# Kernel tuning notes

Hardware: AMD Instinct MI355X
Metric: run time of the kernel (lower is better)

Reference implementation:

```python
import jax, jax.numpy as jnp
import numpy as np

N_HEAD = 12
D_HEAD = 64  # key_dim // n_head = 768 // 12


def sparsemax(z):
    # Martins & Astudillo (2016): projection of each row of z onto the simplex.
    K = z.shape[-1]
    z_sorted = -jnp.sort(-z, axis=-1)                      # descending sort
    cs = jnp.cumsum(z_sorted, axis=-1)
    r = jnp.arange(1, K + 1, dtype=z.dtype)
    support = (1.0 + r * z_sorted) > cs                    # support set indicator
    ksz = jnp.sum(support, axis=-1, keepdims=True)         # support size k(z)
    cs_k = jnp.take_along_axis(cs, ksz.astype(jnp.int32) - 1, axis=-1)
    tau = (cs_k - 1.0) / ksz.astype(z.dtype)               # threshold
    return jnp.maximum(z - tau, 0.0)


def setup_inputs() -> dict:
    key = jax.random.key(0)
    kq, kk, kv, kwq, kbq, kwk, kbk = jax.random.split(key, 7)
    B, L, D = 8, 1024, 768
    scale = 0.02
    return {
        "q": jax.random.normal(kq, (B, L, D), jnp.float32),
        "k": jax.random.normal(kk, (B, L, D), jnp.float32),
        "v": jax.random.normal(kv, (B, L, D), jnp.float32),
        "Wq": jax.random.normal(kwq, (D, D), jnp.float32) * scale,  # torch Linear weight [out,in]
        "bq": jax.random.normal(kbq, (D,), jnp.float32) * scale,
        "Wk": jax.random.normal(kwk, (D, D), jnp.float32) * scale,
        "bk": jax.random.normal(kbk, (D,), jnp.float32) * scale,
    }


def reference(q, k, v, Wq, bq, Wk, bk):
    B, Lq, _ = q.shape
    Lkv = k.shape[1]
    # project and split heads: [B, H, L, d_head]
    qh = (q @ Wq.T + bq).reshape(B, Lq, N_HEAD, D_HEAD).transpose(0, 2, 1, 3)
    kh = (k @ Wk.T + bk).reshape(B, Lkv, N_HEAD, D_HEAD).transpose(0, 2, 1, 3)
    inv_sqrt_d = jnp.asarray(1.0 / np.sqrt(D_HEAD), q.dtype)
    scores = jnp.einsum("bhqd,bhkd->bhqk", qh, kh) * inv_sqrt_d  # [B,H,Lq,Lkv]
    attn = sparsemax(scores)
    attn = attn.mean(axis=1)                                      # head-mean -> [B,Lq,Lkv]
    # eval mode: smooth_max is identity (training-only smoothing)
    output = jnp.einsum("bqk,bkd->bqd", attn, v)                  # [B,Lq,Dv]
    return output, attn
```

## Files before the change

kernel.cpp:

```cpp
#include <hip/hip_runtime.h>

#define BSZ 8
#define NH 12
#define LSEQ 1024
#define DMODEL 768
#define DHEAD 64
#define OUT_ELEMS 6291456
#define ATTN_ELEMS 8388608

typedef __attribute__((ext_vector_type(8))) short short8;
typedef __attribute__((ext_vector_type(4))) float f32x4;

__device__ __forceinline__ int   f2i(float x) { union { float f; int i; } c; c.f = x; return c.i; }
__device__ __forceinline__ float i2f(int x)   { union { int i; float f; } c; c.i = x; return c.f; }

__device__ __forceinline__ unsigned short f2bf(float x) {
    union { float f; unsigned u; } c; c.f = x;
    unsigned r = (c.u + 0x7FFF + ((c.u >> 16) & 1)) >> 16;
    return (unsigned short)r;
}
__device__ __forceinline__ float bf2f(unsigned short h) {
    union { float f; unsigned u; } c; c.u = ((unsigned)h) << 16;
    return c.f;
}
__device__ __forceinline__ void split2(float x, unsigned short& h, unsigned short& l) {
    h = f2bf(x);
    l = f2bf(x - bf2f(h));
}

template<int CTRL>
__device__ __forceinline__ float dppadd(float v) {
    return v + i2f(__builtin_amdgcn_update_dpp(0, f2i(v), CTRL, 0xF, 0xF, true));
}
template<int CTRL>
__device__ __forceinline__ float dppmax(float v) {
    return fmaxf(v, i2f(__builtin_amdgcn_update_dpp(f2i(v), f2i(v), CTRL, 0xF, 0xF, false)));
}

__device__ __forceinline__ void wsum4(float s[4]) {
#define WS(CTRL) _Pragma("unroll") for (int rr = 0; rr < 4; ++rr) { s[rr] = dppadd<CTRL>(s[rr]); }
    WS(0x111) WS(0x112) WS(0x114) WS(0x118) WS(0x142) WS(0x143)
#undef WS
#pragma unroll
    for (int rr = 0; rr < 4; ++rr) s[rr] = i2f(__builtin_amdgcn_readlane(f2i(s[rr]), 63));
}

__device__ __forceinline__ void wsummax4(float s[4], float m[4]) {
#define WS(CTRL) _Pragma("unroll") for (int rr = 0; rr < 4; ++rr) { s[rr] = dppadd<CTRL>(s[rr]); m[rr] = dppmax<CTRL>(m[rr]); }
    WS(0x111) WS(0x112) WS(0x114) WS(0x118) WS(0x142) WS(0x143)
#undef WS
#pragma unroll
    for (int rr = 0; rr < 4; ++rr) {
        s[rr] = i2f(__builtin_amdgcn_readlane(f2i(s[rr]), 63));
        m[rr] = i2f(__builtin_amdgcn_readlane(f2i(m[rr]), 63));
    }
}

__global__ __launch_bounds__(256) void proj_mfma(
    const float* __restrict__ qin, const float* __restrict__ kin,
    const float* __restrict__ Wq, const float* __restrict__ bq,
    const float* __restrict__ Wk, const float* __restrict__ bk,
    unsigned short* __restrict__ ws) {
    const float* A; const float* W; const float* bias;
    unsigned short* hi; unsigned short* lo;
    if (blockIdx.z == 0) { A = qin; W = Wq; bias = bq; hi = ws;                lo = ws + OUT_ELEMS; }
    else                 { A = kin; W = Wk; bias = bk; hi = ws + 2*OUT_ELEMS; lo = ws + 3*OUT_ELEMS; }

    __shared__ unsigned short Ah[128][32], Al[128][32];
    __shared__ unsigned short Bh[128][32], Bl[128][32];

    const int t    = threadIdx.x;
    const int lane = t & 63;
    const int w    = t >> 6;
    const int wr   = w >> 1, wc = w & 1;
    const int mrow = lane & 15, quad = lane >> 4;
    const int m0   = blockIdx.y * 128;
    const int n0   = blockIdx.x * 128;

    const int srow = t >> 3;
    const int scol = (t & 7) * 4;

    f32x4 acc[4][4];
#pragma unroll
    for (int i = 0; i < 4; ++i)
#pragma unroll
        for (int j = 0; j < 4; ++j) acc[i][j] = (f32x4){0.f, 0.f, 0.f, 0.f};

    for (int k0 = 0; k0 < DMODEL; k0 += 32) {
        float4 av[4], wv[4];
#pragma unroll
        for (int i = 0; i < 4; ++i) {
            av[i] = *(const float4*)&A[(size_t)(m0 + srow + i * 32) * DMODEL + k0 + scol];
            wv[i] = *(const float4*)&W[(size_t)(n0 + srow + i * 32) * DMODEL + k0 + scol];
        }
        __syncthreads();
#pragma unroll
        for (int i = 0; i < 4; ++i) {
            ushort4 h4, l4;
            split2(av[i].x, h4.x, l4.x); split2(av[i].y, h4.y, l4.y);
            split2(av[i].z, h4.z, l4.z); split2(av[i].w, h4.w, l4.w);
            *(ushort4*)&Ah[srow + i * 32][scol] = h4;
            *(ushort4*)&Al[srow + i * 32][scol] = l4;
            split2(wv[i].x, h4.x, l4.x); split2(wv[i].y, h4.y, l4.y);
            split2(wv[i].z, h4.z, l4.z); split2(wv[i].w, h4.w, l4.w);
            *(ushort4*)&Bh[srow + i * 32][scol] = h4;
            *(ushort4*)&Bl[srow + i * 32][scol] = l4;
        }
        __syncthreads();

        short8 ah[4], al[4], bh[4], bl[4];
#pragma unroll
        for (int i = 0; i < 4; ++i) {
            ah[i] = *(const short8*)&Ah[wr * 64 + i * 16 + mrow][quad * 8];
            al[i] = *(const short8*)&Al[wr * 64 + i * 16 + mrow][quad * 8];
            bh[i] = *(const short8*)&Bh[wc * 64 + i * 16 + mrow][quad * 8];
            bl[i] = *(const short8*)&Bl[wc * 64 + i * 16 + mrow][quad * 8];
        }
#pragma unroll
        for (int i = 0; i < 4; ++i)
#pragma unroll
            for (int j = 0; j < 4; ++j) {
                acc[i][j] = __builtin_amdgcn_mfma_f32_16x16x32_bf16(al[i], bh[j], acc[i][j], 0, 0, 0);
                acc[i][j] = __builtin_amdgcn_mfma_f32_16x16x32_bf16(ah[i], bl[j], acc[i][j], 0, 0, 0);
                acc[i][j] = __builtin_amdgcn_mfma_f32_16x16x32_bf16(ah[i], bh[j], acc[i][j], 0, 0, 0);
            }
    }

#pragma unroll
    for (int j = 0; j < 4; ++j) {
        const int ng = n0 + wc * 64 + j * 16 + mrow;
        const float bj = bias[ng];
        const int hh = ng >> 6, dd = ng & 63;
#pragma unroll
        for (int i = 0; i < 4; ++i) {
#pragma unroll
            for (int reg = 0; reg < 4; ++reg) {
                const int mg = m0 + wr * 64 + i * 16 + quad * 4 + reg;
                const float c = acc[i][j][reg] + bj;
                unsigned short ch, cl;
                split2(c, ch, cl);
                const size_t idx = (((size_t)(mg >> 10) * NH + hh) * LSEQ + (mg & 1023)) * DHEAD + dd;
                hi[idx] = ch;
                lo[idx] = cl;
            }
        }
    }
}

__global__ __launch_bounds__(256, 2) void attn_kernel(
    const unsigned short* __restrict__ ws, float* __restrict__ attn_out) {
    __shared__ float S[16 * 1024];

    const unsigned short* Qhi = ws;
    const unsigned short* Qlo = ws + OUT_ELEMS;
    const unsigned short* Khi = ws + 2 * OUT_ELEMS;
    const unsigned short* Klo = ws + 3 * OUT_ELEMS;

    const int t = threadIdx.x;
    const int lane = t & 63;
    const int w = t >> 6;
    const int b = blockIdx.y;
    const int q0 = blockIdx.x * 16;

    const int mrow = lane & 15;
    const int quad = lane >> 4;

    f32x4 acc[16];
#pragma unroll
    for (int j = 0; j < 16; ++j) acc[j] = (f32x4){0.f, 0.f, 0.f, 0.f};

    for (int h = 0; h < NH; ++h) {
        const size_t hb = ((size_t)b * NH + h) * (LSEQ * DHEAD);

        const size_t aoff = hb + (size_t)(q0 + mrow) * DHEAD + quad * 8;
        short8 ah0 = *(const short8*)(Qhi + aoff);
        short8 ah1 = *(const short8*)(Qhi + aoff + 32);
        short8 al0 = *(const short8*)(Qlo + aoff);
        short8 al1 = *(const short8*)(Qlo + aoff + 32);

        __syncthreads();

#pragma unroll 4
        for (int nt = 0; nt < 16; ++nt) {
            const int n0 = w * 256 + nt * 16;
            const size_t boff = hb + (size_t)(n0 + mrow) * DHEAD + quad * 8;
            short8 bh0 = *(const short8*)(Khi + boff);
            short8 bh1 = *(const short8*)(Khi + boff + 32);
            short8 bl0 = *(const short8*)(Klo + boff);
            short8 bl1 = *(const short8*)(Klo + boff + 32);
            f32x4 d = {0.f, 0.f, 0.f, 0.f};
            d = __builtin_amdgcn_mfma_f32_16x16x32_bf16(al0, bh0, d, 0, 0, 0);
            d = __builtin_amdgcn_mfma_f32_16x16x32_bf16(ah0, bl0, d, 0, 0, 0);
            d = __builtin_amdgcn_mfma_f32_16x16x32_bf16(ah0, bh0, d, 0, 0, 0);
            d = __builtin_amdgcn_mfma_f32_16x16x32_bf16(al1, bh1, d, 0, 0, 0);
            d = __builtin_amdgcn_mfma_f32_16x16x32_bf16(ah1, bl1, d, 0, 0, 0);
            d = __builtin_amdgcn_mfma_f32_16x16x32_bf16(ah1, bh1, d, 0, 0, 0);
#pragma unroll
            for (int reg = 0; reg < 4; ++reg)
                S[(quad * 4 + reg) * 1024 + n0 + mrow] = d[reg] * 0.125f;
        }
        __syncthreads();

        {
            float z[4][16];
            float sv[4], mv[4];
#pragma unroll
            for (int rr = 0; rr < 4; ++rr) {
                const int r = w * 4 + rr;
#pragma unroll
                for (int c = 0; c < 4; ++c)
                    *(f32x4*)&z[rr][c * 4] = *(const f32x4*)&S[r * 1024 + c * 256 + lane * 4];
                float s = 0.f, m = z[rr][0];
#pragma unroll
                for (int j = 0; j < 16; ++j) s += z[rr][j];
#pragma unroll
                for (int j = 1; j < 16; ++j) m = fmaxf(m, z[rr][j]);
                sv[rr] = s; mv[rr] = m;
            }
            wsummax4(sv, mv);

            float tau[4]; int prev[4]; bool done[4];
#pragma unroll
            for (int rr = 0; rr < 4; ++rr) {
                tau[rr] = fmaxf((sv[rr] - 1.0f) * (1.0f / 1024.0f), mv[rr] - 1.0f);
                prev[rr] = -1; done[rr] = false;
            }

            for (int it = 0; it < 64; ++it) {
                float s4[4]; int c4[4];
#pragma unroll
                for (int rr = 0; rr < 4; ++rr) {
                    float s = 0.f; int c = 0;
#pragma unroll
                    for (int j = 0; j < 16; ++j) {
                        bool gt = z[rr][j] > tau[rr];
                        c += __popcll(__ballot(gt));
                        s += gt ? z[rr][j] : 0.f;
                    }
                    s4[rr] = s; c4[rr] = c;
                }
                wsum4(s4);
                bool alldone = true;
#pragma unroll
                for (int rr = 0; rr < 4; ++rr) {
                    if (!done[rr]) {
                        if (c4[rr] == prev[rr]) done[rr] = true;
                        else { tau[rr] = (s4[rr] - 1.0f) / (float)c4[rr]; prev[rr] = c4[rr]; }
                    }
                    alldone = alldone && done[rr];
                }
                if (alldone) break;
            }

#pragma unroll
            for (int rr = 0; rr < 4; ++rr) {
                const int r = w * 4 + rr;
#pragma unroll
                for (int c = 0; c < 4; ++c) {
                    f32x4 p;
#pragma unroll
                    for (int j = 0; j < 4; ++j)
                        p[j] = fmaxf(z[rr][c * 4 + j] - tau[rr], 0.f);
                    *(f32x4*)&S[r * 1024 + c * 256 + lane * 4] = p;
                }
            }
        }
        __syncthreads();

#pragma unroll
        for (int j = 0; j < 16; ++j) {
            f32x4 vv = *(const f32x4*)&S[j * 1024 + t * 4];
            acc[j] += vv;
        }
    }

    float* ao = attn_out + ((size_t)b * LSEQ + q0) * LSEQ;
#pragma unroll
    for (int j = 0; j < 16; ++j) {
        f32x4 o = acc[j] * (1.0f / 12.0f);
        *(f32x4*)&ao[(size_t)j * LSEQ + t * 4] = o;
    }
}

__global__ __launch_bounds__(256) void out_mfma(
    const float* __restrict__ attn, const float* __restrict__ v,
    float* __restrict__ out) {
    const int b = blockIdx.z;
    const float* Ab = attn + (size_t)b * LSEQ * LSEQ;
    const float* Vb = v    + (size_t)b * LSEQ * DMODEL;
    float* Cb       = out  + (size_t)b * LSEQ * DMODEL;

    __shared__ unsigned short Ah[128][32], Al[128][32];
    __shared__ unsigned short Bh[128][36], Bl[128][36];

    const int t    = threadIdx.x;
    const int lane = t & 63;
    const int w    = t >> 6;
    const int wr   = w >> 1, wc = w & 1;
    const int mrow = lane & 15, quad = lane >> 4;
    const int m0   = blockIdx.y * 128;
    const int n0   = blockIdx.x * 128;

    const int srow = t >> 3;
    const int scol = (t & 7) * 4;
    const int bn   = t & 127;
    const int bk0  = (t >> 7) * 16;

    f32x4 acc[4][4];
#pragma unroll
    for (int i = 0; i < 4; ++i)
#pragma unroll
        for (int j = 0; j < 4; ++j) acc[i][j] = (f32x4){0.f, 0.f, 0.f, 0.f};

    for (int k0 = 0; k0 < LSEQ; k0 += 32) {
        float4 av[4];
#pragma unroll
        for (int i = 0; i < 4; ++i)
            av[i] = *(const float4*)&Ab[(size_t)(m0 + srow + i * 32) * LSEQ + k0 + scol];
        float bv[16];
#pragma unroll
        for (int i = 0; i < 16; ++i)
            bv[i] = Vb[(size_t)(k0 + bk0 + i) * DMODEL + n0 + bn];

        __syncthreads();
#pragma unroll
        for (int i = 0; i < 4; ++i) {
            ushort4 h4, l4;
            split2(av[i].x, h4.x, l4.x); split2(av[i].y, h4.y, l4.y);
            split2(av[i].z, h4.z, l4.z); split2(av[i].w, h4.w, l4.w);
            *(ushort4*)&Ah[srow + i * 32][scol] = h4;
            *(ushort4*)&Al[srow + i * 32][scol] = l4;
        }
#pragma unroll
        for (int g = 0; g < 4; ++g) {
            ushort4 h4, l4;
            split2(bv[g * 4 + 0], h4.x, l4.x); split2(bv[g * 4 + 1], h4.y, l4.y);
            split2(bv[g * 4 + 2], h4.z, l4.z); split2(bv[g * 4 + 3], h4.w, l4.w);
            *(ushort4*)&Bh[bn][bk0 + g * 4] = h4;
            *(ushort4*)&Bl[bn][bk0 + g * 4] = l4;
        }
        __syncthreads();

        short8 ah[4], al[4], bh[4], bl[4];
#pragma unroll
        for (int i = 0; i < 4; ++i) {
            ah[i] = *(const short8*)&Ah[wr * 64 + i * 16 + mrow][quad * 8];
            al[i] = *(const short8*)&Al[wr * 64 + i * 16 + mrow][quad * 8];
        }
#pragma unroll
        for (int j = 0; j < 4; ++j) {
            const unsigned short* ph = &Bh[wc * 64 + j * 16 + mrow][quad * 8];
            const unsigned short* pl = &Bl[wc * 64 + j * 16 + mrow][quad * 8];
            uint2 h0 = *(const uint2*)ph;
            uint2 h1 = *(const uint2*)(ph + 4);
            uint2 l0 = *(const uint2*)pl;
            uint2 l1 = *(const uint2*)(pl + 4);
            union { uint u[4]; short8 s; } ch, cl;
            ch.u[0] = h0.x; ch.u[1] = h0.y; ch.u[2] = h1.x; ch.u[3] = h1.y;
            cl.u[0] = l0.x; cl.u[1] = l0.y; cl.u[2] = l1.x; cl.u[3] = l1.y;
            bh[j] = ch.s; bl[j] = cl.s;
        }
#pragma unroll
        for (int i = 0; i < 4; ++i)
#pragma unroll
            for (int j = 0; j < 4; ++j) {
                acc[i][j] = __builtin_amdgcn_mfma_f32_16x16x32_bf16(al[i], bh[j], acc[i][j], 0, 0, 0);
                acc[i][j] = __builtin_amdgcn_mfma_f32_16x16x32_bf16(ah[i], bl[j], acc[i][j], 0, 0, 0);
                acc[i][j] = __builtin_amdgcn_mfma_f32_16x16x32_bf16(ah[i], bh[j], acc[i][j], 0, 0, 0);
            }
    }

#pragma unroll
    for (int i = 0; i < 4; ++i)
#pragma unroll
        for (int j = 0; j < 4; ++j)
#pragma unroll
            for (int reg = 0; reg < 4; ++reg) {
                const int mg = m0 + wr * 64 + i * 16 + quad * 4 + reg;
                const int ng = n0 + wc * 64 + j * 16 + mrow;
                Cb[(size_t)mg * DMODEL + ng] = acc[i][j][reg];
            }
}

extern "C" void kernel_launch(void* const* d_in, const int* in_sizes, int n_in,
                              void* d_out, int out_size, void* d_ws, size_t ws_size,
                              hipStream_t stream) {
    const float* q  = (const float*)d_in[0];
    const float* k  = (const float*)d_in[1];
    const float* v  = (const float*)d_in[2];
    const float* Wq = (const float*)d_in[3];
    const float* bq = (const float*)d_in[4];
    const float* Wk = (const float*)d_in[5];
    const float* bk = (const float*)d_in[6];

    float* out  = (float*)d_out;
    float* attn = out + OUT_ELEMS;
    unsigned short* ws = (unsigned short*)d_ws;

    hipLaunchKernelGGL(proj_mfma, dim3(6, 64, 2), dim3(256), 0, stream,
                       q, k, Wq, bq, Wk, bk, ws);
    hipLaunchKernelGGL(attn_kernel, dim3(64, 8), dim3(256), 0, stream,
                       ws, attn);
    hipLaunchKernelGGL(out_mfma, dim3(6, 8, 8), dim3(256), 0, stream,
                       attn, v, out);
}
```

Baseline: 554.0 us.

## Shrink attention blocks to 8 query rows and accumulate head-mean in registers

The attention kernel now processes 8 query rows per 128-thread block instead of 16 rows per 256 threads. This halves the shared score buffer, launches twice as many blocks, and keeps the per-head sparsemax output in registers, which removes the write-back to shared memory, one barrier and the final re-read. The 1/sqrt(d) scale moves into the Q projection epilogue, and the sum, max and threshold loops are split into four independent chains to shorten dependency latency. The MFMA work still uses 16 rows with the 8 query rows duplicated, so half of the QK compute is wasted, and the iteration cap for the threshold search drops from 64 to 48.

```diff
diff --git a/kernel.cpp b/kernel.cpp
--- a/kernel.cpp
+++ b/kernel.cpp
@@ -65,6 +65,7 @@
     unsigned short* hi; unsigned short* lo;
     if (blockIdx.z == 0) { A = qin; W = Wq; bias = bq; hi = ws;                lo = ws + OUT_ELEMS; }
     else                 { A = kin; W = Wk; bias = bk; hi = ws + 2*OUT_ELEMS; lo = ws + 3*OUT_ELEMS; }
+    const float oscale = (blockIdx.z == 0) ? 0.125f : 1.0f;
 
     __shared__ unsigned short Ah[128][32], Al[128][32];
     __shared__ unsigned short Bh[128][32], Bl[128][32];
@@ -136,7 +137,7 @@
 #pragma unroll
             for (int reg = 0; reg < 4; ++reg) {
                 const int mg = m0 + wr * 64 + i * 16 + quad * 4 + reg;
-                const float c = acc[i][j][reg] + bj;
+                const float c = (acc[i][j][reg] + bj) * oscale;
                 unsigned short ch, cl;
                 split2(c, ch, cl);
                 const size_t idx = (((size_t)(mg >> 10) * NH + hh) * LSEQ + (mg & 1023)) * DHEAD + dd;
@@ -147,9 +148,9 @@
     }
 }
 
-__global__ __launch_bounds__(256, 2) void attn_kernel(
+__global__ __launch_bounds__(128) void attn_kernel(
     const unsigned short* __restrict__ ws, float* __restrict__ attn_out) {
-    __shared__ float S[16 * 1024];
+    __shared__ float S[8 * 1024];
 
     const unsigned short* Qhi = ws;
     const unsigned short* Qlo = ws + OUT_ELEMS;
@@ -160,19 +161,21 @@
     const int lane = t & 63;
     const int w = t >> 6;
     const int b = blockIdx.y;
-    const int q0 = blockIdx.x * 16;
+    const int q0 = blockIdx.x * 8;
 
     const int mrow = lane & 15;
     const int quad = lane >> 4;
 
-    f32x4 acc[16];
-#pragma unroll
-    for (int j = 0; j < 16; ++j) acc[j] = (f32x4){0.f, 0.f, 0.f, 0.f};
+    f32x4 acc[4][4];
+#pragma unroll
+    for (int rr = 0; rr < 4; ++rr)
+#pragma unroll
+        for (int c = 0; c < 4; ++c) acc[rr][c] = (f32x4){0.f, 0.f, 0.f, 0.f};
 
     for (int h = 0; h < NH; ++h) {
         const size_t hb = ((size_t)b * NH + h) * (LSEQ * DHEAD);
 
-        const size_t aoff = hb + (size_t)(q0 + mrow) * DHEAD + quad * 8;
+        const size_t aoff = hb + (size_t)(q0 + (mrow & 7)) * DHEAD + quad * 8;
         short8 ah0 = *(const short8*)(Qhi + aoff);
         short8 ah1 = *(const short8*)(Qhi + aoff + 32);
         short8 al0 = *(const short8*)(Qlo + aoff);
@@ -181,8 +184,8 @@
         __syncthreads();
 
 #pragma unroll 4
-        for (int nt = 0; nt < 16; ++nt) {
-            const int n0 = w * 256 + nt * 16;
+        for (int nt = 0; nt < 32; ++nt) {
+            const int n0 = w * 512 + nt * 16;
             const size_t boff = hb + (size_t)(n0 + mrow) * DHEAD + quad * 8;
             short8 bh0 = *(const short8*)(Khi + boff);
             short8 bh1 = *(const short8*)(Khi + boff + 32);
@@ -195,9 +198,11 @@
             d = __builtin_amdgcn_mfma_f32_16x16x32_bf16(al1, bh1, d, 0, 0, 0);
             d = __builtin_amdgcn_mfma_f32_16x16x32_bf16(ah1, bl1, d, 0, 0, 0);
             d = __builtin_amdgcn_mfma_f32_16x16x32_bf16(ah1, bh1, d, 0, 0, 0);
-#pragma unroll
-            for (int reg = 0; reg < 4; ++reg)
-                S[(quad * 4 + reg) * 1024 + n0 + mrow] = d[reg] * 0.125f;
+            if (quad < 2) {
+#pragma unroll
+                for (int reg = 0; reg < 4; ++reg)
+                    S[(quad * 4 + reg) * 1024 + n0 + mrow] = d[reg];
+            }
         }
         __syncthreads();
 
@@ -210,12 +215,20 @@
 #pragma unroll
                 for (int c = 0; c < 4; ++c)
                     *(f32x4*)&z[rr][c * 4] = *(const f32x4*)&S[r * 1024 + c * 256 + lane * 4];
-                float s = 0.f, m = z[rr][0];
-#pragma unroll
-                for (int j = 0; j < 16; ++j) s += z[rr][j];
-#pragma unroll
-                for (int j = 1; j < 16; ++j) m = fmaxf(m, z[rr][j]);
-                sv[rr] = s; mv[rr] = m;
+                float s0 = 0.f, s1 = 0.f, s2 = 0.f, s3 = 0.f;
+                float m0 = z[rr][0], m1 = z[rr][1], m2 = z[rr][2], m3 = z[rr][3];
+#pragma unroll
+                for (int j = 0; j < 4; ++j) {
+                    s0 += z[rr][j];      s1 += z[rr][4 + j];
+                    s2 += z[rr][8 + j];  s3 += z[rr][12 + j];
+                }
+#pragma unroll
+                for (int j = 4; j < 16; j += 4) {
+                    m0 = fmaxf(m0, z[rr][j]);     m1 = fmaxf(m1, z[rr][j + 1]);
+                    m2 = fmaxf(m2, z[rr][j + 2]); m3 = fmaxf(m3, z[rr][j + 3]);
+                }
+                sv[rr] = (s0 + s1) + (s2 + s3);
+                mv[rr] = fmaxf(fmaxf(m0, m1), fmaxf(m2, m3));
             }
             wsummax4(sv, mv);
 
@@ -226,18 +239,26 @@
                 prev[rr] = -1; done[rr] = false;
             }
 
-            for (int it = 0; it < 64; ++it) {
+            for (int it = 0; it < 48; ++it) {
                 float s4[4]; int c4[4];
 #pragma unroll
                 for (int rr = 0; rr < 4; ++rr) {
-                    float s = 0.f; int c = 0;
-#pragma unroll
-                    for (int j = 0; j < 16; ++j) {
-                        bool gt = z[rr][j] > tau[rr];
-                        c += __popcll(__ballot(gt));
-                        s += gt ? z[rr][j] : 0.f;
+                    float s0 = 0.f, s1 = 0.f, s2 = 0.f, s3 = 0.f;
+                    int c = 0;
+#pragma unroll
+                    for (int j = 0; j < 4; ++j) {
+                        bool g0 = z[rr][j]      > tau[rr];
+                        bool g1 = z[rr][4 + j]  > tau[rr];
+                        bool g2 = z[rr][8 + j]  > tau[rr];
+                        bool g3 = z[rr][12 + j] > tau[rr];
+                        c += __popcll(__ballot(g0)) + __popcll(__ballot(g1))
+                           + __popcll(__ballot(g2)) + __popcll(__ballot(g3));
+                        s0 += g0 ? z[rr][j]      : 0.f;
+                        s1 += g1 ? z[rr][4 + j]  : 0.f;
+                        s2 += g2 ? z[rr][8 + j]  : 0.f;
+                        s3 += g3 ? z[rr][12 + j] : 0.f;
                     }
-                    s4[rr] = s; c4[rr] = c;
+                    s4[rr] = (s0 + s1) + (s2 + s3); c4[rr] = c;
                 }
                 wsum4(s4);
                 bool alldone = true;
@@ -253,33 +274,23 @@
             }
 
 #pragma unroll
-            for (int rr = 0; rr < 4; ++rr) {
-                const int r = w * 4 + rr;
-#pragma unroll
-                for (int c = 0; c < 4; ++c) {
-                    f32x4 p;
+            for (int rr = 0; rr < 4; ++rr)
+#pragma unroll
+                for (int c = 0; c < 4; ++c)
 #pragma unroll
                     for (int j = 0; j < 4; ++j)
-                        p[j] = fmaxf(z[rr][c * 4 + j] - tau[rr], 0.f);
-                    *(f32x4*)&S[r * 1024 + c * 256 + lane * 4] = p;
-                }
-            }
-        }
-        __syncthreads();
-
-#pragma unroll
-        for (int j = 0; j < 16; ++j) {
-            f32x4 vv = *(const f32x4*)&S[j * 1024 + t * 4];
-            acc[j] += vv;
+                        acc[rr][c][j] += fmaxf(z[rr][c * 4 + j] - tau[rr], 0.f);
         }
     }
 
-    float* ao = attn_out + ((size_t)b * LSEQ + q0) * LSEQ;
-#pragma unroll
-    for (int j = 0; j < 16; ++j) {
-        f32x4 o = acc[j] * (1.0f / 12.0f);
-        *(f32x4*)&ao[(size_t)j * LSEQ + t * 4] = o;
-    }
+    float* ao = attn_out + ((size_t)b * LSEQ + q0 + w * 4) * LSEQ;
+#pragma unroll
+    for (int rr = 0; rr < 4; ++rr)
+#pragma unroll
+        for (int c = 0; c < 4; ++c) {
+            f32x4 o = acc[rr][c] * (1.0f / 12.0f);
+            *(f32x4*)&ao[(size_t)rr * LSEQ + c * 256 + lane * 4] = o;
+        }
 }
 
 __global__ __launch_bounds__(256) void out_mfma(
@@ -399,7 +410,7 @@
 
     hipLaunchKernelGGL(proj_mfma, dim3(6, 64, 2), dim3(256), 0, stream,
                        q, k, Wq, bq, Wk, bk, ws);
-    hipLaunchKernelGGL(attn_kernel, dim3(64, 8), dim3(256), 0, stream,
+    hipLaunchKernelGGL(attn_kernel, dim3(128, 8), dim3(128), 0, stream,
                        ws, attn);
     hipLaunchKernelGGL(out_mfma, dim3(6, 8, 8), dim3(256), 0, stream,
                        attn, v, out);
```

Result: slower. 786.5 us (+42.0%).
